# Performance work log

Hardware: AMD Instinct MI355X
Metric: run time of the kernel (lower is better)

## Reference

```python
import jax, jax.numpy as jnp
import numpy as np

N_NODES = 100000
DEG = 32
T_CH = 16
N_LAYERS = 2


def setup_inputs() -> dict:
    key = jax.random.key(0)
    k0, k1, k2, k3, k4 = jax.random.split(key, 5)
    # every node has exactly DEG outgoing edges -> degrees all = DEG (log finite)
    src = jnp.repeat(jnp.arange(N_NODES, dtype=jnp.int32), DEG)
    dst = jax.random.randint(k0, (N_NODES * DEG,), 0, N_NODES, dtype=jnp.int32)
    edge_index = jnp.stack([src, dst])  # [2, E]
    x = jax.random.normal(k1, (T_CH, N_NODES), dtype=jnp.float32)
    # per-layer scalar params (shared='all' => shape [1,1] each), stacked over layers
    alpha1 = 2.0 * jax.random.uniform(k2, (N_LAYERS, 1, 1), dtype=jnp.float32) - 1.0
    gamma = 2.0 * jax.random.uniform(k3, (N_LAYERS, 1, 1), dtype=jnp.float32) - 1.0
    bias = 2.0 * jax.random.uniform(k4, (N_LAYERS, 1, 1), dtype=jnp.float32) - 1.0
    return {"x": x, "edge_index": edge_index, "alpha1": alpha1, "gamma": gamma, "bias": bias}


def reference(x, edge_index, alpha1, gamma, bias):
    # x: [T, N]; edge_index: [2, E]; params: [L, 1, 1]
    num_nodes = x.shape[-1]
    src, dst = edge_index[0], edge_index[1]
    deg = jnp.zeros((num_nodes,), x.dtype).at[src].add(jnp.ones((), x.dtype))
    log_deg = jnp.log(deg)[None, :]  # [1, N]
    n_layers = alpha1.shape[0]
    for l in range(n_layers):
        a1, g, b = alpha1[l], gamma[l], bias[l]  # each [1, 1]
        degree_power = jax.nn.sigmoid(g)          # fix_gamma=False
        self_w = jnp.exp(a1)
        # NOTE: source's alpha2 property returns alpha1_param for shared='all' (bug kept)
        neigh_w = self_w * jnp.tanh(a1)
        weighted_repr = x * jnp.exp(degree_power * log_deg)  # [T, N]
        # message: x_j (gathered at src) * exp((gp-1)*log_deg[dst]) * edge_weight(=1)
        edge_w = jnp.exp((degree_power - 1.0) * log_deg[:, dst])  # [1, E]
        msgs = x[:, src] * edge_w                                  # [T, E]
        aggr = jnp.zeros_like(x).at[:, dst].add(msgs)              # scatter-add
        x = self_w * weighted_repr + neigh_w * aggr + b            # with_bias=True
    return x
```

## Files before the change

### kernel.cpp

```cpp
#include <hip/hip_runtime.h>
#include <math.h>

#define N_NODES 100000
#define DEG_E   32
#define T_CH    16
#define E_EDGES (N_NODES * DEG_E)

#define BKT_BITS 8
#define NODES_PER_BKT 256
#define NB 391
#define CAP 9216
#define E_TILE 8192
#define NPART ((E_EDGES + E_TILE - 1) / E_TILE)
#define TRANS_BLKS ((N_NODES + 63) / 64)
#define LOG_DEG 3.4657359027997265f

typedef unsigned int uint;
typedef unsigned short ushort;

static __device__ __forceinline__ uint f2bf(float f) {
    uint u = __float_as_uint(f);
    return (u + 0x7fffu + ((u >> 16) & 1u)) >> 16;
}

static __device__ __forceinline__ void addbf(float* a, uint4 w) {
    a[0] += __uint_as_float(w.x << 16);
    a[1] += __uint_as_float(w.x & 0xffff0000u);
    a[2] += __uint_as_float(w.y << 16);
    a[3] += __uint_as_float(w.y & 0xffff0000u);
    a[4] += __uint_as_float(w.z << 16);
    a[5] += __uint_as_float(w.z & 0xffff0000u);
    a[6] += __uint_as_float(w.w << 16);
    a[7] += __uint_as_float(w.w & 0xffff0000u);
}

__global__ void k_front(const float* __restrict__ x, ushort* __restrict__ xt,
                        const int* __restrict__ dst,
                        int* __restrict__ g_cnt, int* __restrict__ ebuf) {
    __shared__ union U {
        float trans[64 * 17];
        struct {
            int cnt[NB]; int off[NB]; int base[NB]; int cur[NB];
            int tile[E_TILE]; int cursor;
        } part;
        __device__ U() {}
    } u;
    int tid = threadIdx.x;

    if (blockIdx.x < TRANS_BLKS) {
        int n0 = blockIdx.x * 64;
        int ni = tid & 63, tq = tid >> 6;
        #pragma unroll
        for (int j = 0; j < 4; ++j) {
            int t = tq * 4 + j;
            int n = n0 + ni;
            if (n < N_NODES) u.trans[ni * 17 + t] = x[t * N_NODES + n];
        }
        __syncthreads();
        uint* xw = (uint*)xt;
        for (int j = tid; j < 512; j += 256) {
            int nl = j >> 3, tp = j & 7;
            int n = n0 + nl;
            if (n < N_NODES) {
                uint lo = f2bf(u.trans[nl * 17 + tp * 2]);
                uint hi = f2bf(u.trans[nl * 17 + tp * 2 + 1]);
                xw[n * 8 + tp] = lo | (hi << 16);
            }
        }
        return;
    }

    int pb = blockIdx.x - TRANS_BLKS;
    for (int i = tid; i < NB; i += 256) u.part.cnt[i] = 0;
    if (tid == 0) u.part.cursor = 0;
    __syncthreads();

    int e0 = pb * E_TILE;
    int n = min(E_TILE, E_EDGES - e0);
    int n4 = n >> 2;
    const int4* d4 = (const int4*)(dst + e0);
    for (int j = tid; j < n4; j += 256) {
        int4 v = d4[j];
        atomicAdd(&u.part.cnt[v.x >> BKT_BITS], 1);
        atomicAdd(&u.part.cnt[v.y >> BKT_BITS], 1);
        atomicAdd(&u.part.cnt[v.z >> BKT_BITS], 1);
        atomicAdd(&u.part.cnt[v.w >> BKT_BITS], 1);
    }
    __syncthreads();
    for (int i = tid; i < NB; i += 256) {
        int c = u.part.cnt[i];
        if (c) {
            u.part.off[i]  = atomicAdd(&u.part.cursor, c);
            u.part.base[i] = CAP * i + atomicAdd(&g_cnt[i], c);
        }
        u.part.cur[i] = 0;
    }
    __syncthreads();
    for (int j = tid; j < n4; j += 256) {
        int4 v = d4[j];
        int de = 4 * j;
        int dd, bkt, p;
        dd = v.x; bkt = dd >> BKT_BITS;
        p = u.part.off[bkt] + atomicAdd(&u.part.cur[bkt], 1);
        u.part.tile[p] = ((de + 0) << 17) | dd;
        dd = v.y; bkt = dd >> BKT_BITS;
        p = u.part.off[bkt] + atomicAdd(&u.part.cur[bkt], 1);
        u.part.tile[p] = ((de + 1) << 17) | dd;
        dd = v.z; bkt = dd >> BKT_BITS;
        p = u.part.off[bkt] + atomicAdd(&u.part.cur[bkt], 1);
        u.part.tile[p] = ((de + 2) << 17) | dd;
        dd = v.w; bkt = dd >> BKT_BITS;
        p = u.part.off[bkt] + atomicAdd(&u.part.cur[bkt], 1);
        u.part.tile[p] = ((de + 3) << 17) | dd;
    }
    __syncthreads();
    for (int j = tid; j < n; j += 256) {
        int v  = u.part.tile[j];
        int de = v >> 17;
        int dd = v & 0x1FFFF;
        int bkt = dd >> BKT_BITS;
        int srcn = (e0 + de) >> 5;
        ebuf[u.part.base[bkt] + (j - u.part.off[bkt])] =
            (srcn << BKT_BITS) | (dd & (NODES_PER_BKT - 1));
    }
}

__global__ __launch_bounds__(512) void k_sg0(
        const int* __restrict__ g_cnt, int* __restrict__ ebuf,
        int* __restrict__ node_info,
        const ushort* __restrict__ xtA, ushort* __restrict__ xtB,
        const float* __restrict__ alpha1, const float* __restrict__ gamma,
        const float* __restrict__ bias) {
    __shared__ int s_pk[CAP];
    __shared__ int s_out[CAP];
    __shared__ int s_cnt[NODES_PER_BKT];
    __shared__ int s_scan[NODES_PER_BKT];
    __shared__ int s_cur[NODES_PER_BKT];
    int b = blockIdx.x;
    int tid = threadIdx.x;
    int base = b * CAP;
    int c = g_cnt[b];

    const int4* v4 = (const int4*)(ebuf + base);
    int c4 = (c + 3) >> 2;
    for (int j = tid; j < c4; j += 512)
        ((int4*)s_pk)[j] = v4[j];
    if (tid < NODES_PER_BKT) s_cnt[tid] = 0;
    __syncthreads();
    for (int j = tid; j < c; j += 512)
        atomicAdd(&s_cnt[s_pk[j] & (NODES_PER_BKT - 1)], 1);
    __syncthreads();

    if (tid < NODES_PER_BKT) s_scan[tid] = s_cnt[tid];
    __syncthreads();
    for (int off = 1; off < NODES_PER_BKT; off <<= 1) {
        int add = 0;
        if (tid < NODES_PER_BKT && tid >= off) add = s_scan[tid - off];
        __syncthreads();
        if (tid < NODES_PER_BKT) s_scan[tid] += add;
        __syncthreads();
    }
    if (tid < NODES_PER_BKT) {
        int excl = s_scan[tid] - s_cnt[tid];
        s_cur[tid] = excl;
        int nn = (b << BKT_BITS) + tid;
        if (nn < N_NODES) node_info[nn] = excl | (s_cnt[tid] << 16);
    }
    __syncthreads();

    for (int j = tid; j < c; j += 512) {
        int pk = s_pk[j];
        int pos = atomicAdd(&s_cur[pk & (NODES_PER_BKT - 1)], 1);
        s_out[pos] = pk >> BKT_BITS;
    }
    __syncthreads();
    for (int j = tid; j < c4; j += 512)
        ((int4*)(ebuf + base))[j] = ((const int4*)s_out)[j];

    int dl = tid >> 1;
    int h  = tid & 1;
    int n  = (b << BKT_BITS) + dl;
    int cnt = s_cnt[dl];
    int st  = s_scan[dl] - cnt;

    const uint4* xv = (const uint4*)xtA;
    float acc[8] = {0.f, 0.f, 0.f, 0.f, 0.f, 0.f, 0.f, 0.f};
    int i = st, end = st + cnt;
    for (; i + 4 <= end; i += 4) {
        int s0 = s_out[i],     s1 = s_out[i + 1];
        int s2 = s_out[i + 2], s3 = s_out[i + 3];
        uint4 w0 = xv[s0 * 2 + h];
        uint4 w1 = xv[s1 * 2 + h];
        uint4 w2 = xv[s2 * 2 + h];
        uint4 w3 = xv[s3 * 2 + h];
        addbf(acc, w0); addbf(acc, w1); addbf(acc, w2); addbf(acc, w3);
    }
    for (; i < end; ++i) {
        uint4 w = xv[s_out[i] * 2 + h];
        addbf(acc, w);
    }

    if (n < N_NODES) {
        float a1 = alpha1[0];
        float gm = gamma[0];
        float bb = bias[0];
        float dp = 1.0f / (1.0f + __expf(-gm));
        float sw = __expf(a1);
        float nw = sw * tanhf(a1);
        float c_self = sw * __expf(dp * LOG_DEG);
        float c_nei  = nw * __expf((dp - 1.0f) * LOG_DEG);

        float self[8] = {0.f, 0.f, 0.f, 0.f, 0.f, 0.f, 0.f, 0.f};
        uint4 swd = xv[n * 2 + h];
        addbf(self, swd);

        float o[8];
        #pragma unroll
        for (int k = 0; k < 8; ++k)
            o[k] = c_self * self[k] + c_nei * acc[k] + bb;

        uint4 w;
        w.x = f2bf(o[0]) | (f2bf(o[1]) << 16);
        w.y = f2bf(o[2]) | (f2bf(o[3]) << 16);
        w.z = f2bf(o[4]) | (f2bf(o[5]) << 16);
        w.w = f2bf(o[6]) | (f2bf(o[7]) << 16);
        ((uint4*)xtB)[n * 2 + h] = w;
    }
}

__global__ void k_gather1(const ushort* __restrict__ xt,
                          const int* __restrict__ node_info,
                          const int* __restrict__ csr,
                          const float* __restrict__ alpha1,
                          const float* __restrict__ gamma,
                          const float* __restrict__ bias,
                          float* __restrict__ out) {
    int tid = blockIdx.x * blockDim.x + threadIdx.x;
    int n = tid >> 3;
    int sub = tid & 7;
    int h = sub & 1;
    int ep = sub >> 1;
    if (n >= N_NODES) return;

    int info = node_info[n];
    int st = (n >> BKT_BITS) * CAP + (info & 0xffff);
    int c  = info >> 16;

    const uint4* xv = (const uint4*)xt;
    float acc[8] = {0.f, 0.f, 0.f, 0.f, 0.f, 0.f, 0.f, 0.f};
    int i = ep;
    for (; i + 12 < c; i += 16) {
        int s0 = csr[st + i],     s1 = csr[st + i + 4];
        int s2 = csr[st + i + 8], s3 = csr[st + i + 12];
        uint4 w0 = xv[s0 * 2 + h];
        uint4 w1 = xv[s1 * 2 + h];
        uint4 w2 = xv[s2 * 2 + h];
        uint4 w3 = xv[s3 * 2 + h];
        addbf(acc, w0); addbf(acc, w1); addbf(acc, w2); addbf(acc, w3);
    }
    for (; i < c; i += 4) {
        uint4 w = xv[csr[st + i] * 2 + h];
        addbf(acc, w);
    }

    #pragma unroll
    for (int k = 0; k < 8; ++k) {
        acc[k] += __shfl_xor(acc[k], 2, 64);
        acc[k] += __shfl_xor(acc[k], 4, 64);
    }

    if (ep == 0) {
        float a1 = alpha1[1];
        float gm = gamma[1];
        float bb = bias[1];
        float dp = 1.0f / (1.0f + __expf(-gm));
        float sw = __expf(a1);
        float nw = sw * tanhf(a1);
        float c_self = sw * __expf(dp * LOG_DEG);
        float c_nei  = nw * __expf((dp - 1.0f) * LOG_DEG);

        float self[8] = {0.f, 0.f, 0.f, 0.f, 0.f, 0.f, 0.f, 0.f};
        uint4 swd = xv[n * 2 + h];
        addbf(self, swd);

        int ch0 = h * 8;
        #pragma unroll
        for (int k = 0; k < 8; ++k)
            out[(ch0 + k) * N_NODES + n] = c_self * self[k] + c_nei * acc[k] + bb;
    }
}

extern "C" void kernel_launch(void* const* d_in, const int* in_sizes, int n_in,
                              void* d_out, int out_size, void* d_ws, size_t ws_size,
                              hipStream_t stream) {
    const float* x      = (const float*)d_in[0];
    const int*   ei     = (const int*)d_in[1];
    const float* alpha1 = (const float*)d_in[2];
    const float* gamma  = (const float*)d_in[3];
    const float* bias   = (const float*)d_in[4];
    float* out = (float*)d_out;
    const int* dst = ei + E_EDGES;

    const int NT = N_NODES * T_CH;
    ushort* xtA      = (ushort*)d_ws;
    ushort* xtB      = xtA + NT;
    int*   ebuf      = (int*)(xtB + NT);
    int*   node_info = ebuf + NB * CAP;
    int*   g_cnt     = node_info + N_NODES;

    const int B = 256;
    hipMemsetAsync(g_cnt, 0, NB * sizeof(int), stream);
    k_front<<<TRANS_BLKS + NPART, B, 0, stream>>>(x, xtA, dst, g_cnt, ebuf);
    k_sg0<<<NB, 512, 0, stream>>>(g_cnt, ebuf, node_info, xtA, xtB,
                                  alpha1, gamma, bias);
    const int grid_g = (N_NODES * 8 + B - 1) / B;
    k_gather1<<<grid_g, B, 0, stream>>>(xtB, node_info, ebuf,
                                        alpha1, gamma, bias, out);
}
```

Before: 154.4 us.

## Fuse three kernels into one cooperative persistent kernel with grid syncs

Merges the partition/transpose front kernel, the layer-0 sort-and-gather kernel and the layer-1 gather kernel into a single cooperative launch of 391 blocks of 512 threads, with grid.sync() between the phases. Each block partitions one edge tile and converts strided transpose tiles, then sorts its bucket and computes layer 0, then runs a grid-stride layer-1 gather. This removes the launch gaps between kernels. In exchange it caps parallelism at 391 blocks, which may underfill the GPU in the partition and gather phases, and it adds the cost of the grid barriers.

```diff
diff --git a/kernel.cpp b/kernel.cpp
--- a/kernel.cpp
+++ b/kernel.cpp
@@ -1,5 +1,8 @@
 #include <hip/hip_runtime.h>
+#include <hip/hip_cooperative_groups.h>
 #include <math.h>
+
+namespace cg = cooperative_groups;
 
 #define N_NODES 100000
 #define DEG_E   32
@@ -11,9 +14,9 @@
 #define NB 391
 #define CAP 9216
 #define E_TILE 8192
-#define NPART ((E_EDGES + E_TILE - 1) / E_TILE)
-#define TRANS_BLKS ((N_NODES + 63) / 64)
+#define TTILES 782
 #define LOG_DEG 3.4657359027997265f
+#define D_UNITS (N_NODES * 8)
 
 typedef unsigned int uint;
 typedef unsigned short ushort;
@@ -34,259 +37,258 @@
     a[7] += __uint_as_float(w.w & 0xffff0000u);
 }
 
-__global__ void k_front(const float* __restrict__ x, ushort* __restrict__ xt,
-                        const int* __restrict__ dst,
-                        int* __restrict__ g_cnt, int* __restrict__ ebuf) {
-    __shared__ union U {
-        float trans[64 * 17];
-        struct {
-            int cnt[NB]; int off[NB]; int base[NB]; int cur[NB];
-            int tile[E_TILE]; int cursor;
-        } part;
-        __device__ U() {}
+__global__ __launch_bounds__(512, 4) void k_all(
+        const float* __restrict__ x, ushort* __restrict__ xtA,
+        ushort* __restrict__ xtB, const int* __restrict__ dst,
+        int* __restrict__ g_cnt, int* __restrict__ ebuf,
+        int* __restrict__ node_info,
+        const float* __restrict__ alpha1, const float* __restrict__ gamma,
+        const float* __restrict__ bias, float* __restrict__ out) {
+    __shared__ union SU {
+        struct { float t[128 * 17]; } a;
+        struct { int cnt[NB], off[NB], base[NB], cur[NB];
+                 int tile[E_TILE]; int cursor; } b;
+        struct { int pk[CAP]; int outv[CAP];
+                 int cnt[NODES_PER_BKT]; int scan[NODES_PER_BKT];
+                 int cur[NODES_PER_BKT]; } c;
+        __device__ SU() {}
     } u;
+    cg::grid_group grid = cg::this_grid();
     int tid = threadIdx.x;
-
-    if (blockIdx.x < TRANS_BLKS) {
-        int n0 = blockIdx.x * 64;
-        int ni = tid & 63, tq = tid >> 6;
-        #pragma unroll
-        for (int j = 0; j < 4; ++j) {
-            int t = tq * 4 + j;
-            int n = n0 + ni;
-            if (n < N_NODES) u.trans[ni * 17 + t] = x[t * N_NODES + n];
-        }
-        __syncthreads();
-        uint* xw = (uint*)xt;
-        for (int j = tid; j < 512; j += 256) {
-            int nl = j >> 3, tp = j & 7;
-            int n = n0 + nl;
-            if (n < N_NODES) {
-                uint lo = f2bf(u.trans[nl * 17 + tp * 2]);
-                uint hi = f2bf(u.trans[nl * 17 + tp * 2 + 1]);
-                xw[n * 8 + tp] = lo | (hi << 16);
-            }
-        }
-        return;
+    int b = blockIdx.x;
+
+    {
+        for (int i = tid; i < NB; i += 512) u.b.cnt[i] = 0;
+        if (tid == 0) u.b.cursor = 0;
+        __syncthreads();
+        int e0 = b * E_TILE;
+        int n = min(E_TILE, E_EDGES - e0);
+        int n4 = n >> 2;
+        const int4* d4 = (const int4*)(dst + e0);
+        for (int j = tid; j < n4; j += 512) {
+            int4 v = d4[j];
+            atomicAdd(&u.b.cnt[v.x >> BKT_BITS], 1);
+            atomicAdd(&u.b.cnt[v.y >> BKT_BITS], 1);
+            atomicAdd(&u.b.cnt[v.z >> BKT_BITS], 1);
+            atomicAdd(&u.b.cnt[v.w >> BKT_BITS], 1);
+        }
+        __syncthreads();
+        for (int i = tid; i < NB; i += 512) {
+            int c = u.b.cnt[i];
+            if (c) {
+                u.b.off[i]  = atomicAdd(&u.b.cursor, c);
+                u.b.base[i] = CAP * i + atomicAdd(&g_cnt[i], c);
+            }
+            u.b.cur[i] = 0;
+        }
+        __syncthreads();
+        for (int j = tid; j < n4; j += 512) {
+            int4 v = d4[j];
+            int de = 4 * j;
+            int dd, bkt, p;
+            dd = v.x; bkt = dd >> BKT_BITS;
+            p = u.b.off[bkt] + atomicAdd(&u.b.cur[bkt], 1);
+            u.b.tile[p] = ((de + 0) << 17) | dd;
+            dd = v.y; bkt = dd >> BKT_BITS;
+            p = u.b.off[bkt] + atomicAdd(&u.b.cur[bkt], 1);
+            u.b.tile[p] = ((de + 1) << 17) | dd;
+            dd = v.z; bkt = dd >> BKT_BITS;
+            p = u.b.off[bkt] + atomicAdd(&u.b.cur[bkt], 1);
+            u.b.tile[p] = ((de + 2) << 17) | dd;
+            dd = v.w; bkt = dd >> BKT_BITS;
+            p = u.b.off[bkt] + atomicAdd(&u.b.cur[bkt], 1);
+            u.b.tile[p] = ((de + 3) << 17) | dd;
+        }
+        __syncthreads();
+        for (int j = tid; j < n; j += 512) {
+            int v  = u.b.tile[j];
+            int de = v >> 17;
+            int dd = v & 0x1FFFF;
+            int bkt = dd >> BKT_BITS;
+            int srcn = (e0 + de) >> 5;
+            ebuf[u.b.base[bkt] + (j - u.b.off[bkt])] =
+                (srcn << BKT_BITS) | (dd & (NODES_PER_BKT - 1));
+        }
+        __syncthreads();
+
+        for (int tile = b; tile < TTILES; tile += NB) {
+            int n0 = tile * 128;
+            int ni = tid & 127, tq = tid >> 7;
+            #pragma unroll
+            for (int j = 0; j < 4; ++j) {
+                int t = tq * 4 + j;
+                int nn = n0 + ni;
+                if (nn < N_NODES) u.a.t[ni * 17 + t] = x[t * N_NODES + nn];
+            }
+            __syncthreads();
+            uint* xw = (uint*)xtA;
+            for (int j = tid; j < 1024; j += 512) {
+                int nl = j >> 3, tp = j & 7;
+                int nn = n0 + nl;
+                if (nn < N_NODES) {
+                    uint lo = f2bf(u.a.t[nl * 17 + tp * 2]);
+                    uint hi = f2bf(u.a.t[nl * 17 + tp * 2 + 1]);
+                    xw[nn * 8 + tp] = lo | (hi << 16);
+                }
+            }
+            __syncthreads();
+        }
     }
-
-    int pb = blockIdx.x - TRANS_BLKS;
-    for (int i = tid; i < NB; i += 256) u.part.cnt[i] = 0;
-    if (tid == 0) u.part.cursor = 0;
-    __syncthreads();
-
-    int e0 = pb * E_TILE;
-    int n = min(E_TILE, E_EDGES - e0);
-    int n4 = n >> 2;
-    const int4* d4 = (const int4*)(dst + e0);
-    for (int j = tid; j < n4; j += 256) {
-        int4 v = d4[j];
-        atomicAdd(&u.part.cnt[v.x >> BKT_BITS], 1);
-        atomicAdd(&u.part.cnt[v.y >> BKT_BITS], 1);
-        atomicAdd(&u.part.cnt[v.z >> BKT_BITS], 1);
-        atomicAdd(&u.part.cnt[v.w >> BKT_BITS], 1);
-    }
-    __syncthreads();
-    for (int i = tid; i < NB; i += 256) {
-        int c = u.part.cnt[i];
-        if (c) {
-            u.part.off[i]  = atomicAdd(&u.part.cursor, c);
-            u.part.base[i] = CAP * i + atomicAdd(&g_cnt[i], c);
-        }
-        u.part.cur[i] = 0;
-    }
-    __syncthreads();
-    for (int j = tid; j < n4; j += 256) {
-        int4 v = d4[j];
-        int de = 4 * j;
-        int dd, bkt, p;
-        dd = v.x; bkt = dd >> BKT_BITS;
-        p = u.part.off[bkt] + atomicAdd(&u.part.cur[bkt], 1);
-        u.part.tile[p] = ((de + 0) << 17) | dd;
-        dd = v.y; bkt = dd >> BKT_BITS;
-        p = u.part.off[bkt] + atomicAdd(&u.part.cur[bkt], 1);
-        u.part.tile[p] = ((de + 1) << 17) | dd;
-        dd = v.z; bkt = dd >> BKT_BITS;
-        p = u.part.off[bkt] + atomicAdd(&u.part.cur[bkt], 1);
-        u.part.tile[p] = ((de + 2) << 17) | dd;
-        dd = v.w; bkt = dd >> BKT_BITS;
-        p = u.part.off[bkt] + atomicAdd(&u.part.cur[bkt], 1);
-        u.part.tile[p] = ((de + 3) << 17) | dd;
-    }
-    __syncthreads();
-    for (int j = tid; j < n; j += 256) {
-        int v  = u.part.tile[j];
-        int de = v >> 17;
-        int dd = v & 0x1FFFF;
-        int bkt = dd >> BKT_BITS;
-        int srcn = (e0 + de) >> 5;
-        ebuf[u.part.base[bkt] + (j - u.part.off[bkt])] =
-            (srcn << BKT_BITS) | (dd & (NODES_PER_BKT - 1));
-    }
-}
-
-__global__ __launch_bounds__(512) void k_sg0(
-        const int* __restrict__ g_cnt, int* __restrict__ ebuf,
-        int* __restrict__ node_info,
-        const ushort* __restrict__ xtA, ushort* __restrict__ xtB,
-        const float* __restrict__ alpha1, const float* __restrict__ gamma,
-        const float* __restrict__ bias) {
-    __shared__ int s_pk[CAP];
-    __shared__ int s_out[CAP];
-    __shared__ int s_cnt[NODES_PER_BKT];
-    __shared__ int s_scan[NODES_PER_BKT];
-    __shared__ int s_cur[NODES_PER_BKT];
-    int b = blockIdx.x;
-    int tid = threadIdx.x;
-    int base = b * CAP;
-    int c = g_cnt[b];
-
-    const int4* v4 = (const int4*)(ebuf + base);
-    int c4 = (c + 3) >> 2;
-    for (int j = tid; j < c4; j += 512)
-        ((int4*)s_pk)[j] = v4[j];
-    if (tid < NODES_PER_BKT) s_cnt[tid] = 0;
-    __syncthreads();
-    for (int j = tid; j < c; j += 512)
-        atomicAdd(&s_cnt[s_pk[j] & (NODES_PER_BKT - 1)], 1);
-    __syncthreads();
-
-    if (tid < NODES_PER_BKT) s_scan[tid] = s_cnt[tid];
-    __syncthreads();
-    for (int off = 1; off < NODES_PER_BKT; off <<= 1) {
-        int add = 0;
-        if (tid < NODES_PER_BKT && tid >= off) add = s_scan[tid - off];
-        __syncthreads();
-        if (tid < NODES_PER_BKT) s_scan[tid] += add;
-        __syncthreads();
-    }
-    if (tid < NODES_PER_BKT) {
-        int excl = s_scan[tid] - s_cnt[tid];
-        s_cur[tid] = excl;
-        int nn = (b << BKT_BITS) + tid;
-        if (nn < N_NODES) node_info[nn] = excl | (s_cnt[tid] << 16);
-    }
-    __syncthreads();
-
-    for (int j = tid; j < c; j += 512) {
-        int pk = s_pk[j];
-        int pos = atomicAdd(&s_cur[pk & (NODES_PER_BKT - 1)], 1);
-        s_out[pos] = pk >> BKT_BITS;
-    }
-    __syncthreads();
-    for (int j = tid; j < c4; j += 512)
-        ((int4*)(ebuf + base))[j] = ((const int4*)s_out)[j];
-
-    int dl = tid >> 1;
-    int h  = tid & 1;
-    int n  = (b << BKT_BITS) + dl;
-    int cnt = s_cnt[dl];
-    int st  = s_scan[dl] - cnt;
-
-    const uint4* xv = (const uint4*)xtA;
-    float acc[8] = {0.f, 0.f, 0.f, 0.f, 0.f, 0.f, 0.f, 0.f};
-    int i = st, end = st + cnt;
-    for (; i + 4 <= end; i += 4) {
-        int s0 = s_out[i],     s1 = s_out[i + 1];
-        int s2 = s_out[i + 2], s3 = s_out[i + 3];
-        uint4 w0 = xv[s0 * 2 + h];
-        uint4 w1 = xv[s1 * 2 + h];
-        uint4 w2 = xv[s2 * 2 + h];
-        uint4 w3 = xv[s3 * 2 + h];
-        addbf(acc, w0); addbf(acc, w1); addbf(acc, w2); addbf(acc, w3);
-    }
-    for (; i < end; ++i) {
-        uint4 w = xv[s_out[i] * 2 + h];
-        addbf(acc, w);
-    }
-
-    if (n < N_NODES) {
+    grid.sync();
+
+    {
+        int base = b * CAP;
+        int c = g_cnt[b];
+        const int4* v4 = (const int4*)(ebuf + base);
+        int c4 = (c + 3) >> 2;
+        for (int j = tid; j < c4; j += 512)
+            ((int4*)u.c.pk)[j] = v4[j];
+        if (tid < NODES_PER_BKT) u.c.cnt[tid] = 0;
+        __syncthreads();
+        for (int j = tid; j < c; j += 512)
+            atomicAdd(&u.c.cnt[u.c.pk[j] & (NODES_PER_BKT - 1)], 1);
+        __syncthreads();
+
+        if (tid < NODES_PER_BKT) u.c.scan[tid] = u.c.cnt[tid];
+        __syncthreads();
+        for (int off = 1; off < NODES_PER_BKT; off <<= 1) {
+            int add = 0;
+            if (tid < NODES_PER_BKT && tid >= off) add = u.c.scan[tid - off];
+            __syncthreads();
+            if (tid < NODES_PER_BKT) u.c.scan[tid] += add;
+            __syncthreads();
+        }
+        if (tid < NODES_PER_BKT) {
+            int excl = u.c.scan[tid] - u.c.cnt[tid];
+            u.c.cur[tid] = excl;
+            int nn = (b << BKT_BITS) + tid;
+            if (nn < N_NODES) node_info[nn] = excl | (u.c.cnt[tid] << 16);
+        }
+        __syncthreads();
+
+        for (int j = tid; j < c; j += 512) {
+            int pk = u.c.pk[j];
+            int pos = atomicAdd(&u.c.cur[pk & (NODES_PER_BKT - 1)], 1);
+            u.c.outv[pos] = pk >> BKT_BITS;
+        }
+        __syncthreads();
+        for (int j = tid; j < c4; j += 512)
+            ((int4*)(ebuf + base))[j] = ((const int4*)u.c.outv)[j];
+
         float a1 = alpha1[0];
         float gm = gamma[0];
         float bb = bias[0];
-        float dp = 1.0f / (1.0f + __expf(-gm));
+        float dpw = 1.0f / (1.0f + __expf(-gm));
         float sw = __expf(a1);
         float nw = sw * tanhf(a1);
-        float c_self = sw * __expf(dp * LOG_DEG);
-        float c_nei  = nw * __expf((dp - 1.0f) * LOG_DEG);
-
-        float self[8] = {0.f, 0.f, 0.f, 0.f, 0.f, 0.f, 0.f, 0.f};
-        uint4 swd = xv[n * 2 + h];
-        addbf(self, swd);
-
-        float o[8];
-        #pragma unroll
-        for (int k = 0; k < 8; ++k)
-            o[k] = c_self * self[k] + c_nei * acc[k] + bb;
-
-        uint4 w;
-        w.x = f2bf(o[0]) | (f2bf(o[1]) << 16);
-        w.y = f2bf(o[2]) | (f2bf(o[3]) << 16);
-        w.z = f2bf(o[4]) | (f2bf(o[5]) << 16);
-        w.w = f2bf(o[6]) | (f2bf(o[7]) << 16);
-        ((uint4*)xtB)[n * 2 + h] = w;
+        float c_self = sw * __expf(dpw * LOG_DEG);
+        float c_nei  = nw * __expf((dpw - 1.0f) * LOG_DEG);
+
+        int dl = tid >> 1;
+        int h  = tid & 1;
+        int n  = (b << BKT_BITS) + dl;
+        int cnt = u.c.cnt[dl];
+        int st  = u.c.scan[dl] - cnt;
+
+        const uint4* xv = (const uint4*)xtA;
+        float acc[8] = {0.f, 0.f, 0.f, 0.f, 0.f, 0.f, 0.f, 0.f};
+        int i = st, end = st + cnt;
+        for (; i + 4 <= end; i += 4) {
+            int s0 = u.c.outv[i],     s1 = u.c.outv[i + 1];
+            int s2 = u.c.outv[i + 2], s3 = u.c.outv[i + 3];
+            uint4 w0 = xv[s0 * 2 + h];
+            uint4 w1 = xv[s1 * 2 + h];
+            uint4 w2 = xv[s2 * 2 + h];
+            uint4 w3 = xv[s3 * 2 + h];
+            addbf(acc, w0); addbf(acc, w1); addbf(acc, w2); addbf(acc, w3);
+        }
+        for (; i < end; ++i) {
+            uint4 w = xv[u.c.outv[i] * 2 + h];
+            addbf(acc, w);
+        }
+
+        if (n < N_NODES) {
+            float self[8] = {0.f, 0.f, 0.f, 0.f, 0.f, 0.f, 0.f, 0.f};
+            uint4 swd = xv[n * 2 + h];
+            addbf(self, swd);
+
+            float o[8];
+            #pragma unroll
+            for (int k = 0; k < 8; ++k)
+                o[k] = c_self * self[k] + c_nei * acc[k] + bb;
+
+            uint4 w;
+            w.x = f2bf(o[0]) | (f2bf(o[1]) << 16);
+            w.y = f2bf(o[2]) | (f2bf(o[3]) << 16);
+            w.z = f2bf(o[4]) | (f2bf(o[5]) << 16);
+            w.w = f2bf(o[6]) | (f2bf(o[7]) << 16);
+            ((uint4*)xtB)[n * 2 + h] = w;
+        }
     }
-}
-
-__global__ void k_gather1(const ushort* __restrict__ xt,
-                          const int* __restrict__ node_info,
-                          const int* __restrict__ csr,
-                          const float* __restrict__ alpha1,
-                          const float* __restrict__ gamma,
-                          const float* __restrict__ bias,
-                          float* __restrict__ out) {
-    int tid = blockIdx.x * blockDim.x + threadIdx.x;
-    int n = tid >> 3;
-    int sub = tid & 7;
-    int h = sub & 1;
-    int ep = sub >> 1;
-    if (n >= N_NODES) return;
-
-    int info = node_info[n];
-    int st = (n >> BKT_BITS) * CAP + (info & 0xffff);
-    int c  = info >> 16;
-
-    const uint4* xv = (const uint4*)xt;
-    float acc[8] = {0.f, 0.f, 0.f, 0.f, 0.f, 0.f, 0.f, 0.f};
-    int i = ep;
-    for (; i + 12 < c; i += 16) {
-        int s0 = csr[st + i],     s1 = csr[st + i + 4];
-        int s2 = csr[st + i + 8], s3 = csr[st + i + 12];
-        uint4 w0 = xv[s0 * 2 + h];
-        uint4 w1 = xv[s1 * 2 + h];
-        uint4 w2 = xv[s2 * 2 + h];
-        uint4 w3 = xv[s3 * 2 + h];
-        addbf(acc, w0); addbf(acc, w1); addbf(acc, w2); addbf(acc, w3);
-    }
-    for (; i < c; i += 4) {
-        uint4 w = xv[csr[st + i] * 2 + h];
-        addbf(acc, w);
-    }
-
-    #pragma unroll
-    for (int k = 0; k < 8; ++k) {
-        acc[k] += __shfl_xor(acc[k], 2, 64);
-        acc[k] += __shfl_xor(acc[k], 4, 64);
-    }
-
-    if (ep == 0) {
+    grid.sync();
+
+    {
         float a1 = alpha1[1];
         float gm = gamma[1];
         float bb = bias[1];
-        float dp = 1.0f / (1.0f + __expf(-gm));
+        float dpw = 1.0f / (1.0f + __expf(-gm));
         float sw = __expf(a1);
         float nw = sw * tanhf(a1);
-        float c_self = sw * __expf(dp * LOG_DEG);
-        float c_nei  = nw * __expf((dp - 1.0f) * LOG_DEG);
-
-        float self[8] = {0.f, 0.f, 0.f, 0.f, 0.f, 0.f, 0.f, 0.f};
-        uint4 swd = xv[n * 2 + h];
-        addbf(self, swd);
-
-        int ch0 = h * 8;
-        #pragma unroll
-        for (int k = 0; k < 8; ++k)
-            out[(ch0 + k) * N_NODES + n] = c_self * self[k] + c_nei * acc[k] + bb;
+        float c_self = sw * __expf(dpw * LOG_DEG);
+        float c_nei  = nw * __expf((dpw - 1.0f) * LOG_DEG);
+
+        const uint4* xv = (const uint4*)xtB;
+        const int stride = NB * 512;
+        for (int ui = b * 512 + tid; ; ui += stride) {
+            bool live = (ui < D_UNITS);
+            int n = ui >> 3;
+            int sub = ui & 7;
+            int h = sub & 1;
+            int ep = sub >> 1;
+
+            float acc[8] = {0.f, 0.f, 0.f, 0.f, 0.f, 0.f, 0.f, 0.f};
+            if (live) {
+                int info = node_info[n];
+                int st = (n >> BKT_BITS) * CAP + (info & 0xffff);
+                int c  = info >> 16;
+                const int* csr = ebuf;
+                int i = st + ep;
+                int end = st + c;
+                for (; i + 12 < end; i += 16) {
+                    int s0 = csr[i],     s1 = csr[i + 4];
+                    int s2 = csr[i + 8], s3 = csr[i + 12];
+                    uint4 w0 = xv[s0 * 2 + h];
+                    uint4 w1 = xv[s1 * 2 + h];
+                    uint4 w2 = xv[s2 * 2 + h];
+                    uint4 w3 = xv[s3 * 2 + h];
+                    addbf(acc, w0); addbf(acc, w1); addbf(acc, w2); addbf(acc, w3);
+                }
+                for (; i < end; i += 4) {
+                    uint4 w = xv[csr[i] * 2 + h];
+                    addbf(acc, w);
+                }
+            }
+
+            #pragma unroll
+            for (int k = 0; k < 8; ++k) {
+                acc[k] += __shfl_xor(acc[k], 2, 64);
+                acc[k] += __shfl_xor(acc[k], 4, 64);
+            }
+
+            if (live && ep == 0) {
+                float self[8] = {0.f, 0.f, 0.f, 0.f, 0.f, 0.f, 0.f, 0.f};
+                uint4 swd = xv[n * 2 + h];
+                addbf(self, swd);
+
+                int ch0 = h * 8;
+                #pragma unroll
+                for (int k = 0; k < 8; ++k)
+                    out[(ch0 + k) * N_NODES + n] =
+                        c_self * self[k] + c_nei * acc[k] + bb;
+            }
+            if (ui + stride >= D_UNITS + stride) break;
+            if (ui >= D_UNITS) break;
+        }
     }
 }
 
@@ -308,12 +310,10 @@
     int*   node_info = ebuf + NB * CAP;
     int*   g_cnt     = node_info + N_NODES;
 
-    const int B = 256;
     hipMemsetAsync(g_cnt, 0, NB * sizeof(int), stream);
-    k_front<<<TRANS_BLKS + NPART, B, 0, stream>>>(x, xtA, dst, g_cnt, ebuf);
-    k_sg0<<<NB, 512, 0, stream>>>(g_cnt, ebuf, node_info, xtA, xtB,
-                                  alpha1, gamma, bias);
-    const int grid_g = (N_NODES * 8 + B - 1) / B;
-    k_gather1<<<grid_g, B, 0, stream>>>(xtB, node_info, ebuf,
-                                        alpha1, gamma, bias, out);
+
+    void* args[] = {(void*)&x, (void*)&xtA, (void*)&xtB, (void*)&dst,
+                    (void*)&g_cnt, (void*)&ebuf, (void*)&node_info,
+                    (void*)&alpha1, (void*)&gamma, (void*)&bias, (void*)&out};
+    hipLaunchCooperativeKernel((void*)k_all, dim3(NB), dim3(512), args, 0, stream);
 }
```

Measured after the change: 273.3 us. +77.0%, slower.
